# Kernel optimization log

Hardware: AMD Instinct MI355X
Metric: run time of the kernel (lower is better)

The kernel has to match this reference:

```python
import jax, jax.numpy as jnp
import numpy as np

# Model constants (from source: model_dim=1024, head_dim=128, num_heads=8)
L = 8          # num layers (reduced from 16 for tractable reference memory)
T = 2048       # packed tokens, B == 1 (varlen)
DIM = 1024
NH = 8
NKV = 4        # GQA kv heads
HD = 128
KVD = NKV * HD
BLOCK = 128
WS = 3
WIN = WS * BLOCK           # sliding-window size for 'S' layers
ATTN_SCALE = 0.12
PATTERN = 'SSSL'
GATE_CH = 32
EPS = 1.1920929e-07        # torch F.rms_norm default eps = finfo(fp32).eps


def rms_norm(x):
    return x * jax.lax.rsqrt(jnp.mean(x * x, axis=-1, keepdims=True) + EPS)


def apply_rotary(x, cos, sin):
    # x: [T, H, HD]; cos/sin: [T, 1, HD//2]
    d = x.shape[-1] // 2
    x1, x2 = x[..., :d], x[..., d:]
    return jnp.concatenate([x1 * cos + x2 * sin, -x1 * sin + x2 * cos], axis=-1)


def has_ve(layer_idx, n_layer):
    return layer_idx % 2 == (n_layer - 1) % 2


def setup_inputs() -> dict:
    key = jax.random.key(0)
    ks = jax.random.split(key, 9)
    x = jax.random.normal(ks[0], (1, T, DIM), jnp.float32)
    ve = jax.random.normal(ks[1], (L, T, KVD), jnp.float32)
    s = DIM ** -0.5
    Wq = jax.random.normal(ks[2], (L, DIM, NH * HD), jnp.float32) * s
    Wk = jax.random.normal(ks[3], (L, DIM, KVD), jnp.float32) * s
    Wv = jax.random.normal(ks[4], (L, DIM, KVD), jnp.float32) * s
    Wo = jax.random.normal(ks[5], (L, NH * HD, DIM), jnp.float32) * (NH * HD) ** -0.5
    Wgate = jax.random.normal(ks[6], (L, GATE_CH, NKV), jnp.float32) * GATE_CH ** -0.5
    Wfc = jax.random.normal(ks[7], (L, DIM, 4 * DIM), jnp.float32) * s
    Wproj = jax.random.normal(ks[8], (L, 4 * DIM, DIM), jnp.float32) * (4 * DIM) ** -0.5
    # RoPE tables (absolute positions of the packed batch, as in the source)
    inv_freq = 1.0 / (10000.0 ** (jnp.arange(HD // 2, dtype=jnp.float32) / (HD // 2)))
    ang = jnp.arange(T, dtype=jnp.float32)[:, None] * inv_freq[None, :]
    cos = jnp.cos(ang)[:, None, :]
    sin = jnp.sin(ang)[:, None, :]
    # cu_seqlens: 4 packed documents of 512 tokens
    seqlens = jnp.array([0, 512, 1024, 1536, 2048], dtype=jnp.int32)
    return dict(x=x, ve=ve, Wq=Wq, Wk=Wk, Wv=Wv, Wo=Wo, Wgate=Wgate,
                Wfc=Wfc, Wproj=Wproj, cos=cos, sin=sin, seqlens=seqlens)


def reference(x, ve, Wq, Wk, Wv, Wo, Wgate, Wfc, Wproj, cos, sin, seqlens):
    h = x[0]  # [T, DIM], B == 1 (varlen packing)
    pos = jnp.arange(T)
    doc = jnp.searchsorted(seqlens, pos, side='right') - 1
    diff = pos[:, None] - pos[None, :]
    base = (diff >= 0) & (doc[:, None] == doc[None, :])   # causal within doc
    mask_S = base & (diff <= WIN)                         # sliding window
    neg = jnp.float32(-1e30)
    rep = NH // NKV
    for l in range(L):
        xn = rms_norm(h)
        q = (xn @ Wq[l]).reshape(T, NH, HD)
        k = (xn @ Wk[l]).reshape(T, NKV, HD)
        v = (xn @ Wv[l]).reshape(T, NKV, HD)
        if has_ve(l, L):
            gate = 2.0 * jax.nn.sigmoid(xn[:, :GATE_CH] @ Wgate[l])  # [T, NKV]
            v = v + gate[:, :, None] * ve[l].reshape(T, NKV, HD)
        q = rms_norm(apply_rotary(q, cos, sin))
        k = rms_norm(apply_rotary(k, cos, sin))
        k = jnp.repeat(k, rep, axis=1)   # GQA -> full heads
        v2 = jnp.repeat(v, rep, axis=1)
        scores = jnp.einsum('thd,shd->hts', q, k) * ATTN_SCALE  # [NH, T, T]
        mask = mask_S if PATTERN[l % len(PATTERN)] == 'S' else base
        scores = jnp.where(mask[None], scores, neg)
        p = jax.nn.softmax(scores, axis=-1)
        y = jnp.einsum('hts,shd->thd', p, v2).reshape(T, NH * HD)
        h = h + y @ Wo[l]
        m = jnp.square(jax.nn.relu(rms_norm(h) @ Wfc[l]))  # relu(x)^2 MLP
        h = h + m @ Wproj[l]
    return h[None]
```

## Files before the change

kernel.cpp:

```cpp
#include <hip/hip_runtime.h>
#include <hip/hip_bf16.h>
#include <cstdint>
#include <cstddef>

#define TT     2048
#define DMODEL 1024
#define NHQ    8
#define HD     128
#define KVD    512
#define WIN    384
#define EPSF   1.1920929e-07f
#define SCALE  0.12f

typedef __attribute__((ext_vector_type(8))) short bf16x8;
typedef __attribute__((ext_vector_type(4))) float f32x4;

#define WAITV(N)  asm volatile("s_waitcnt vmcnt(" #N ")" ::: "memory")

__device__ __forceinline__ float b2f(unsigned short u) {
    unsigned int i = ((unsigned int)u) << 16; float f; __builtin_memcpy(&f, &i, 4); return f;
}
__device__ __forceinline__ unsigned short f2b(float f) {
    unsigned int i; __builtin_memcpy(&i, &f, 4);
    unsigned int r = (i + 0x7fffu + ((i >> 16) & 1u)) >> 16;
    return (unsigned short)r;
}

__device__ __forceinline__ void gl_lds16(const unsigned short* g, unsigned short* l) {
    __builtin_amdgcn_global_load_lds(
        (const __attribute__((address_space(1))) unsigned int*)g,
        (__attribute__((address_space(3))) unsigned int*)l, 16, 0, 0);
}
__device__ __forceinline__ void gl_lds16f(const float* g, float* l) {
    __builtin_amdgcn_global_load_lds(
        (const __attribute__((address_space(1))) unsigned int*)g,
        (__attribute__((address_space(3))) unsigned int*)l, 16, 0, 0);
}

__global__ __launch_bounds__(512)
void convT_k(const float* __restrict__ Wq, const float* __restrict__ Wk,
             const float* __restrict__ Wv, const float* __restrict__ Wo,
             const float* __restrict__ Wfc, const float* __restrict__ Wproj,
             unsigned short* __restrict__ Bqkv, unsigned short* __restrict__ Bo,
             unsigned short* __restrict__ Bfc, unsigned short* __restrict__ Bproj)
{
    __shared__ float lt[128 * 128];
    const int bid = blockIdx.x, tid = threadIdx.x, l = blockIdx.y;

    const float* W; unsigned short* Wt; int K, N, t, nbase;
    if (bid < 64)         { W = Wq    + (size_t)l * 1024 * 1024; Wt = Bqkv  + (size_t)l * 2048 * 1024; K = 1024; N = 1024; t = bid;       nbase = 0;    }
    else if (bid < 96)    { W = Wk    + (size_t)l * 1024 * 512;  Wt = Bqkv  + (size_t)l * 2048 * 1024; K = 1024; N = 512;  t = bid - 64;  nbase = 1024; }
    else if (bid < 128)   { W = Wv    + (size_t)l * 1024 * 512;  Wt = Bqkv  + (size_t)l * 2048 * 1024; K = 1024; N = 512;  t = bid - 96;  nbase = 1536; }
    else if (bid < 192)   { W = Wo    + (size_t)l * 1024 * 1024; Wt = Bo    + (size_t)l * 1024 * 1024; K = 1024; N = 1024; t = bid - 128; nbase = 0;    }
    else if (bid < 448)   { W = Wfc   + (size_t)l * 1024 * 4096; Wt = Bfc   + (size_t)l * 4096 * 1024; K = 1024; N = 4096; t = bid - 192; nbase = 0;    }
    else                  { W = Wproj + (size_t)l * 4096 * 1024; Wt = Bproj + (size_t)l * 1024 * 4096; K = 4096; N = 1024; t = bid - 448; nbase = 0;    }

    const int ktiles = K >> 7;
    const int kt0 = (t % ktiles) * 128, nt0 = (t / ktiles) * 128;

    const int lane = tid & 63, w = tid >> 6;
    const int lhi = lane >> 5;
    const int lc  = lane & 31;

    #pragma unroll
    for (int rd = 0; rd < 8; ++rd) {
        const int k = rd * 16 + w * 2 + lhi;
        const int csrc = lc ^ ((k >> 3) & 31);
        const float* src = W + (size_t)(kt0 + k) * N + nt0 + csrc * 4;
        float* dst = lt + (size_t)(rd * 16 + w * 2) * 128;
        gl_lds16f(src, dst);
    }
    __syncthreads();

    #pragma unroll
    for (int i = 0; i < 4; ++i) {
        int flat = i * 512 + tid;
        int n = flat >> 4, kc = (flat & 15) * 8;
        const int c = ((n >> 2) ^ (kc >> 3)) & 31;
        const float* rp = lt + (size_t)kc * 128 + c * 4 + (n & 3);
        unsigned short o[8];
        #pragma unroll
        for (int j = 0; j < 8; ++j) o[j] = f2b(rp[j * 128]);
        *(uint4*)(Wt + (size_t)(nbase + nt0 + n) * K + kt0 + kc) = *(const uint4*)o;
    }
}

template<int EPI>
__global__ __launch_bounds__(256, 2)
void gemm4(const unsigned short* __restrict__ A, const unsigned short* __restrict__ Bt,
           unsigned short* __restrict__ Cp, int K, int ksplit, int Ntot)
{
    __shared__ unsigned short As[2 * 128 * 64];
    __shared__ unsigned short Bs[2 * 128 * 64];
    const int BUF = 128 * 64;
    const int tid = threadIdx.x, lane = tid & 63, wv = tid >> 6;

    const int gx = gridDim.x;
    const int nwg = gx * gridDim.y;
    const int ihw = blockIdx.y * gx + blockIdx.x;
    const int q = nwg >> 3, r = nwg & 7;
    const int xcd = ihw & 7, pos = ihw >> 3;
    const int lg = (xcd < r) ? xcd * (q + 1) + pos
                             : r * (q + 1) + (xcd - r) * q + pos;
    const int m0 = (lg % gx) * 128, n0 = (lg / gx) * 128;

    const int kbeg = blockIdx.z * ksplit;
    const int NT = ksplit >> 6;

    const int wr = (wv >> 1) * 64, wc = (wv & 1) * 64;
    const int l15 = lane & 15, g = lane >> 4;
    const int srow = lane >> 3;
    const int sxor = (((lane & 7) ^ srow) << 3);

    const unsigned short* gA0 = A  + (size_t)(m0 + wv * 32 + srow) * K + sxor;
    const unsigned short* gB0 = Bt + (size_t)(n0 + wv * 32 + srow) * K + sxor;

    auto stage = [&](int t) {
        const int b = t & 1;
        const size_t k = (size_t)kbeg + ((size_t)t << 6);
        unsigned short* la = As + b * BUF + (wv * 32) * 64;
        unsigned short* lb = Bs + b * BUF + (wv * 32) * 64;
        #pragma unroll
        for (int c = 0; c < 4; ++c) {
            gl_lds16(gA0 + (size_t)(c * 8) * K + k, la + c * 8 * 64);
            gl_lds16(gB0 + (size_t)(c * 8) * K + k, lb + c * 8 * 64);
        }
    };

    f32x4 acc[4][4] = {};

    stage(0);
    for (int t = 0; t < NT; ++t) {
        if (t + 1 < NT) { stage(t + 1); WAITV(8); }
        else            { WAITV(0); }
        __builtin_amdgcn_s_barrier();

        const unsigned short* Ac = As + (t & 1) * BUF;
        const unsigned short* Bc = Bs + (t & 1) * BUF;
        bf16x8 af[4][2], bfv[4][2];
        #pragma unroll
        for (int mi = 0; mi < 4; ++mi) {
            const int row = wr + mi * 16 + l15, x = row & 7;
            #pragma unroll
            for (int kk = 0; kk < 2; ++kk)
                af[mi][kk] = *(const bf16x8*)(Ac + row * 64 + (((kk * 4 + g) ^ x) << 3));
        }
        #pragma unroll
        for (int ni = 0; ni < 4; ++ni) {
            const int row = wc + ni * 16 + l15, x = row & 7;
            #pragma unroll
            for (int kk = 0; kk < 2; ++kk)
                bfv[ni][kk] = *(const bf16x8*)(Bc + row * 64 + (((kk * 4 + g) ^ x) << 3));
        }
        __builtin_amdgcn_s_setprio(1);
        #pragma unroll
        for (int kk = 0; kk < 2; ++kk)
            #pragma unroll
            for (int mi = 0; mi < 4; ++mi)
                #pragma unroll
                for (int ni = 0; ni < 4; ++ni)
                    acc[mi][ni] = __builtin_amdgcn_mfma_f32_16x16x32_bf16(af[mi][kk], bfv[ni][kk], acc[mi][ni], 0, 0, 0);
        __builtin_amdgcn_s_setprio(0);
        __builtin_amdgcn_s_barrier();
    }

    const int lr4 = (lane >> 4) * 4;
    unsigned short* Cz = Cp + (size_t)blockIdx.z * TT * Ntot;
    #pragma unroll
    for (int mi = 0; mi < 4; ++mi)
        #pragma unroll
        for (int ni = 0; ni < 4; ++ni)
            #pragma unroll
            for (int r2 = 0; r2 < 4; ++r2) {
                int row = m0 + wr + mi * 16 + lr4 + r2;
                int col = n0 + wc + ni * 16 + l15;
                size_t idx = (size_t)row * Ntot + col;
                float v = acc[mi][ni][r2];
                if (EPI == 0) Cz[idx] = f2b(v);
                else {
                    float z = v > 0.f ? v * v : 0.f;
                    Cz[idx] = f2b(z);
                }
            }
}

__global__ __launch_bounds__(256)
void rmsnormF_k(float* __restrict__ h, const unsigned short* __restrict__ part, int nz,
                unsigned short* __restrict__ xn)
{
    const int t = blockIdx.x, tid = threadIdx.x;
    const size_t idx = (size_t)t * (DMODEL / 4) + tid;
    float4 v = ((const float4*)h)[idx];
    for (int z = 0; z < nz; ++z) {
        ushort4 p = ((const ushort4*)part)[idx + (size_t)z * (TT * DMODEL / 4)];
        v.x += b2f(p.x); v.y += b2f(p.y); v.z += b2f(p.z); v.w += b2f(p.w);
    }
    if (nz > 0) ((float4*)h)[idx] = v;

    float ss = v.x*v.x + v.y*v.y + v.z*v.z + v.w*v.w;
    #pragma unroll
    for (int m = 1; m < 64; m <<= 1) ss += __shfl_xor(ss, m);
    __shared__ float red[4];
    if ((tid & 63) == 0) red[tid >> 6] = ss;
    __syncthreads();
    float tot = red[0] + red[1] + red[2] + red[3];
    float rs = rsqrtf(tot * (1.f / DMODEL) + EPSF);
    unsigned short o[4] = { f2b(v.x*rs), f2b(v.y*rs), f2b(v.z*rs), f2b(v.w*rs) };
    *(ushort4*)(xn + (size_t)t * DMODEL + tid * 4) = *(const ushort4*)o;
}

__global__ __launch_bounds__(256)
void reduce_add_k(float* __restrict__ h, const unsigned short* __restrict__ part, int nz)
{
    const int i = blockIdx.x * 256 + threadIdx.x;
    float4 hv = ((float4*)h)[i];
    for (int z = 0; z < nz; ++z) {
        ushort4 p = ((const ushort4*)part)[i + (size_t)z * (TT * DMODEL / 4)];
        hv.x += b2f(p.x); hv.y += b2f(p.y); hv.z += b2f(p.z); hv.w += b2f(p.w);
    }
    ((float4*)h)[i] = hv;
}

__global__ __launch_bounds__(256)
void post_qkv_k(const unsigned short* __restrict__ qkv, const unsigned short* __restrict__ xn,
                const float* __restrict__ cosb, const float* __restrict__ sinb,
                const float* __restrict__ Wgate, const float* __restrict__ vel, int hasve,
                unsigned short* __restrict__ qn, unsigned short* __restrict__ kn,
                unsigned short* __restrict__ vrow)
{
    const size_t S2 = (size_t)TT * 2048;
    const int t = blockIdx.x, tid = threadIdx.x;
    __shared__ float cs[64], sn[64], gate[4];
    if (tid < 64) { cs[tid] = cosb[t * 64 + tid]; sn[tid] = sinb[t * 64 + tid]; }
    if (hasve && tid >= 64 && tid < 68) {
        int g = tid - 64; float a = 0.f;
        for (int c = 0; c < 32; ++c) a += b2f(xn[(size_t)t * DMODEL + c]) * Wgate[c * 4 + g];
        gate[g] = 2.f / (1.f + __expf(-a));
    }
    __syncthreads();
    if (tid < 96) {
        const int hid = tid >> 3, sub = tid & 7;
        const unsigned short* src; unsigned short* dst;
        if (hid < 8) { src = qkv + (size_t)t * 2048 + hid * 128;              dst = qn + (size_t)t * 1024 + hid * 128; }
        else         { src = qkv + (size_t)t * 2048 + 1024 + (hid - 8) * 128; dst = kn + (size_t)t * 512 + (hid - 8) * 128; }
        float o1[8], o2[8], ssum = 0.f;
        #pragma unroll
        for (int j = 0; j < 8; ++j) {
            int jj = sub * 8 + j;
            float x1 = b2f(src[jj])      + b2f(src[jj + S2]);
            float x2 = b2f(src[jj + 64]) + b2f(src[jj + 64 + S2]);
            float c = cs[jj], s = sn[jj];
            o1[j] = x1 * c + x2 * s;
            o2[j] = -x1 * s + x2 * c;
            ssum += o1[j]*o1[j] + o2[j]*o2[j];
        }
        ssum += __shfl_xor(ssum, 1); ssum += __shfl_xor(ssum, 2); ssum += __shfl_xor(ssum, 4);
        float rs = rsqrtf(ssum * (1.f / HD) + EPSF);
        #pragma unroll
        for (int j = 0; j < 8; ++j) {
            int jj = sub * 8 + j;
            dst[jj]      = f2b(o1[j] * rs);
            dst[jj + 64] = f2b(o2[j] * rs);
        }
    }
    {
        int d0 = tid * 2;
        #pragma unroll
        for (int j = 0; j < 2; ++j) {
            int d = d0 + j;
            size_t off = (size_t)t * 2048 + 1536 + d;
            float vv = b2f(qkv[off]) + b2f(qkv[off + S2]);
            if (hasve) vv += gate[d >> 7] * vel[(size_t)t * KVD + d];
            vrow[(size_t)t * KVD + d] = f2b(vv);
        }
    }
}

__global__ __launch_bounds__(256)
void vtrans_k(const unsigned short* __restrict__ vrow, unsigned short* __restrict__ vt)
{
    __shared__ unsigned short lt[64][72];
    const int t0 = blockIdx.x * 64, c0 = blockIdx.y * 64, tid = threadIdx.x;
    #pragma unroll
    for (int i = 0; i < 2; ++i) {
        int r = (tid >> 3) + i * 32;
        int c = (tid & 7) * 8;
        bf16x8 v = *(const bf16x8*)(vrow + (size_t)(t0 + r) * KVD + c0 + c);
        #pragma unroll
        for (int j = 0; j < 8; ++j) lt[c + j][r] = ((unsigned short*)&v)[j];
    }
    __syncthreads();
    #pragma unroll
    for (int i = 0; i < 2; ++i) {
        int r = (tid >> 3) + i * 32;
        int c = (tid & 7) * 8;
        *(bf16x8*)(vt + (size_t)(c0 + r) * TT + t0 + c) = *(const bf16x8*)(&lt[r][c]);
    }
}

__global__ __launch_bounds__(256)
void attn_k(const unsigned short* __restrict__ qn, const unsigned short* __restrict__ kn,
            const unsigned short* __restrict__ vt, unsigned short* __restrict__ y,
            const int* __restrict__ seqlens, int isS)
{
    __shared__ float Ot[4][16][132];
    const int tid = threadIdx.x, w = tid >> 6, lane = tid & 63;
    const int h = blockIdx.y, hkv = h >> 1;
    const int qr = (blockIdx.x * 4 + w) * 16;
    const int s1 = seqlens[1], s2 = seqlens[2], s3 = seqlens[3];
    const int l15 = lane & 15, g = lane >> 4;

    bf16x8 qf[4];
    #pragma unroll
    for (int kk = 0; kk < 4; ++kk)
        qf[kk] = *(const bf16x8*)(qn + (size_t)(qr + l15) * 1024 + h * HD + kk * 32 + g * 8);

    const int row = qr + l15;
    const int drow = (row >= s1) + (row >= s2) + (row >= s3);

    int dq = (qr >= s1) + (qr >= s2) + (qr >= s3);
    int dstart = dq == 0 ? 0 : (dq == 1 ? s1 : (dq == 2 ? s2 : s3));
    int smin = dstart;
    if (isS) { int wlo = qr - WIN; if (wlo > smin) smin = wlo; }
    if (smin < 0) smin = 0;
    const int smax = qr + 16;

    f32x4 acc[8] = {};
    float mrow = -1e30f, lrow = 0.f;

    for (int s0 = smin & ~31; s0 < smax; s0 += 32) {
        f32x4 S[2] = {};
        __builtin_amdgcn_s_setprio(1);
        #pragma unroll
        for (int nb = 0; nb < 2; ++nb) {
            int srow = s0 + nb * 16 + l15;
            #pragma unroll
            for (int kk = 0; kk < 4; ++kk) {
                bf16x8 kf = *(const bf16x8*)(kn + (size_t)srow * KVD + hkv * HD + kk * 32 + g * 8);
                S[nb] = __builtin_amdgcn_mfma_f32_16x16x32_bf16(kf, qf[kk], S[nb], 0, 0, 0);
            }
        }
        __builtin_amdgcn_s_setprio(0);

        float sv[2][4];
        #pragma unroll
        for (int nb = 0; nb < 2; ++nb)
            #pragma unroll
            for (int r = 0; r < 4; ++r) {
                int s = s0 + nb * 16 + 4 * g + r;
                int dcol = (s >= s1) + (s >= s2) + (s >= s3);
                bool valid = (s <= row) && (dcol == drow) && (!isS || (row - s) <= WIN);
                sv[nb][r] = valid ? S[nb][r] * SCALE : -1e30f;
            }

        float pm = sv[0][0];
        #pragma unroll
        for (int r = 1; r < 4; ++r) pm = fmaxf(pm, sv[0][r]);
        #pragma unroll
        for (int r = 0; r < 4; ++r) pm = fmaxf(pm, sv[1][r]);
        pm = fmaxf(pm, __shfl_xor(pm, 16));
        pm = fmaxf(pm, __shfl_xor(pm, 32));
        float mnew = fmaxf(mrow, pm);
        float scl2 = __expf(mrow - mnew);
        float p0[4], p1[4], ps = 0.f;
        #pragma unroll
        for (int r = 0; r < 4; ++r) {
            p0[r] = __expf(sv[0][r] - mnew);
            p1[r] = __expf(sv[1][r] - mnew);
            ps += p0[r] + p1[r];
        }
        ps += __shfl_xor(ps, 16);
        ps += __shfl_xor(ps, 32);
        lrow = lrow * scl2 + ps;
        mrow = mnew;
        #pragma unroll
        for (int nb2 = 0; nb2 < 8; ++nb2) acc[nb2] *= scl2;

        unsigned short pt[8];
        const int base = l15 + ((g & 1) << 5);
        #pragma unroll
        for (int jh = 0; jh < 2; ++jh)
            #pragma unroll
            for (int r = 0; r < 4; ++r) {
                float ta = __shfl(p0[r], base + 16 * jh);
                float tb = __shfl(p1[r], base + 16 * jh);
                pt[jh * 4 + r] = f2b(g >= 2 ? tb : ta);
            }
        bf16x8 pf;
        #pragma unroll
        for (int j = 0; j < 8; ++j) ((unsigned short*)&pf)[j] = pt[j];

        __builtin_amdgcn_s_setprio(1);
        #pragma unroll
        for (int nb2 = 0; nb2 < 8; ++nb2) {
            bf16x8 vf = *(const bf16x8*)(vt + (size_t)(hkv * HD + nb2 * 16 + l15) * TT + s0 + g * 8);
            acc[nb2] = __builtin_amdgcn_mfma_f32_16x16x32_bf16(vf, pf, acc[nb2], 0, 0, 0);
        }
        __builtin_amdgcn_s_setprio(0);
    }

    const float inv = 1.f / lrow;
    #pragma unroll
    for (int nb2 = 0; nb2 < 8; ++nb2)
        #pragma unroll
        for (int r = 0; r < 4; ++r)
            Ot[w][l15][nb2 * 16 + 4 * g + r] = acc[nb2][r] * inv;
    __syncthreads();
    const int qo = lane >> 2, dblk = (lane & 3) * 32;
    #pragma unroll
    for (int i4 = 0; i4 < 4; ++i4) {
        unsigned short ob[8];
        #pragma unroll
        for (int j = 0; j < 8; ++j) ob[j] = f2b(Ot[w][qo][dblk + i4 * 8 + j]);
        *(uint4*)(y + (size_t)(qr + qo) * 1024 + h * HD + dblk + i4 * 8) = *(const uint4*)ob;
    }
}

extern "C" void kernel_launch(void* const* d_in, const int* in_sizes, int n_in,
                              void* d_out, int out_size, void* d_ws, size_t ws_size,
                              hipStream_t stream)
{
    const float* x       = (const float*)d_in[0];
    const float* ve      = (const float*)d_in[1];
    const float* Wq      = (const float*)d_in[2];
    const float* Wk      = (const float*)d_in[3];
    const float* Wv      = (const float*)d_in[4];
    const float* Wo      = (const float*)d_in[5];
    const float* Wgate   = (const float*)d_in[6];
    const float* Wfc     = (const float*)d_in[7];
    const float* Wproj   = (const float*)d_in[8];
    const float* cosb    = (const float*)d_in[9];
    const float* sinb    = (const float*)d_in[10];
    const int*   seqlens = (const int*)d_in[11];

    float* h = (float*)d_out;
    char* ws = (char*)d_ws;
    unsigned short* xn    = (unsigned short*)(ws);
    unsigned short* qn    = (unsigned short*)(ws + (4ull  << 20));
    unsigned short* kn    = (unsigned short*)(ws + (8ull  << 20));
    unsigned short* vrow  = (unsigned short*)(ws + (10ull << 20));
    unsigned short* vt    = (unsigned short*)(ws + (12ull << 20));
    unsigned short* yb    = (unsigned short*)(ws + (14ull << 20));
    unsigned short* mb    = (unsigned short*)(ws + (18ull << 20));
    unsigned short* part  = (unsigned short*)(ws + (34ull << 20));
    unsigned short* Bqkv  = (unsigned short*)(ws + (50ull  << 20));
    unsigned short* Bo    = (unsigned short*)(ws + (82ull  << 20));
    unsigned short* Bfc   = (unsigned short*)(ws + (98ull  << 20));
    unsigned short* Bproj = (unsigned short*)(ws + (162ull << 20));

    hipMemcpyAsync(h, x, (size_t)TT * DMODEL * sizeof(float), hipMemcpyDeviceToDevice, stream);

    convT_k<<<dim3(704, 8), 512, 0, stream>>>(Wq, Wk, Wv, Wo, Wfc, Wproj,
                                              Bqkv, Bo, Bfc, Bproj);

    for (int l = 0; l < 8; ++l) {
        int hasve = (l % 2) == 1;
        int isS   = (l % 4) != 3;

        rmsnormF_k<<<TT, 256, 0, stream>>>(h, part, l == 0 ? 0 : 4, xn);

        gemm4<0><<<dim3(16, 16, 2), 256, 0, stream>>>(xn, Bqkv + (size_t)l * 2048 * 1024,
                                                      part, 1024, 512, 2048);

        post_qkv_k<<<TT, 256, 0, stream>>>(part, xn, cosb, sinb,
            Wgate + (size_t)l * 128, ve + (size_t)l * TT * KVD, hasve, qn, kn, vrow);

        vtrans_k<<<dim3(32, 8), 256, 0, stream>>>(vrow, vt);

        attn_k<<<dim3(32, 8), 256, 0, stream>>>(qn, kn, vt, yb, seqlens, isS);

        gemm4<0><<<dim3(16, 8, 4), 256, 0, stream>>>(yb, Bo + (size_t)l * 1024 * 1024,
                                                     part, 1024, 256, 1024);

        rmsnormF_k<<<TT, 256, 0, stream>>>(h, part, 4, xn);

        gemm4<2><<<dim3(16, 32, 1), 256, 0, stream>>>(xn, Bfc + (size_t)l * 4096 * 1024,
                                                      mb, 1024, 1024, 4096);

        gemm4<0><<<dim3(16, 8, 4), 256, 0, stream>>>(mb, Bproj + (size_t)l * 1024 * 4096,
                                                     part, 4096, 1024, 1024);
    }

    reduce_add_k<<<2048, 256, 0, stream>>>(h, part, 4);
}
```

Before: 1.388 ms.

## Add 256x128-tile 8-wave GEMM kernel for the MLP fc and proj matmuls

Adds a new gemm9 kernel that uses 512-thread workgroups and 256x128 output tiles, double-buffered in LDS. The A tile is staged in two 128-row halves interleaved with the MFMA compute, and workgroups are remapped so neighbouring tiles land on the same XCD. The MLP up-projection and down-projection now launch through it instead of gemm4. The aim is more data reuse per tile and better overlap of global loads with compute. The cost is higher register and LDS use, which leaves one workgroup per CU, and only half as many workgroups per launch.

```diff
diff --git a/kernel.cpp b/kernel.cpp
--- a/kernel.cpp
+++ b/kernel.cpp
@@ -164,7 +164,6 @@
         __builtin_amdgcn_s_barrier();
     }
 
-    const int lr4 = (lane >> 4) * 4;
     unsigned short* Cz = Cp + (size_t)blockIdx.z * TT * Ntot;
     #pragma unroll
     for (int mi = 0; mi < 4; ++mi)
@@ -172,8 +171,142 @@
         for (int ni = 0; ni < 4; ++ni)
             #pragma unroll
             for (int r2 = 0; r2 < 4; ++r2) {
-                int row = m0 + wr + mi * 16 + lr4 + r2;
+                int row = m0 + wr + mi * 16 + g * 4 + r2;
                 int col = n0 + wc + ni * 16 + l15;
+                size_t idx = (size_t)row * Ntot + col;
+                float v = acc[mi][ni][r2];
+                if (EPI == 0) Cz[idx] = f2b(v);
+                else {
+                    float z = v > 0.f ? v * v : 0.f;
+                    Cz[idx] = f2b(z);
+                }
+            }
+}
+
+template<int EPI>
+__global__ __launch_bounds__(512, 1)
+void gemm9(const unsigned short* __restrict__ A, const unsigned short* __restrict__ Bt,
+           unsigned short* __restrict__ Cp, int K, int ksplit, int Ntot)
+{
+    __shared__ unsigned short As[2 * 2 * 128 * 64];
+    __shared__ unsigned short Bs[2 * 128 * 64];
+    const int HBUF = 128 * 64;
+    const int tid = threadIdx.x, lane = tid & 63, wv = tid >> 6;
+    const int wm = wv >> 2, wn = wv & 3;
+
+    const int gx = gridDim.x;
+    const int nwg = gx * gridDim.y;
+    const int ihw = blockIdx.y * gx + blockIdx.x;
+    const int q = nwg >> 3, r = nwg & 7;
+    const int xcd = ihw & 7, pos = ihw >> 3;
+    const int lg = (xcd < r) ? xcd * (q + 1) + pos
+                             : r * (q + 1) + (xcd - r) * q + pos;
+    const int m0 = (lg % gx) * 256, n0 = (lg / gx) * 128;
+
+    const int kbeg = blockIdx.z * ksplit;
+    const int NT = ksplit >> 6;
+
+    const int l15 = lane & 15, g = lane >> 4;
+    const int srow = tid >> 3;
+    const int sxor = (((tid & 7) ^ (srow & 7)) << 3);
+
+    const unsigned short* gA = A  + (size_t)(m0 + srow) * K + sxor;
+    const unsigned short* gB = Bt + (size_t)(n0 + srow) * K + sxor;
+
+    auto stageA = [&](int t, int mh) {
+        const int buf = t & 1;
+        const size_t kof = (size_t)kbeg + ((size_t)t << 6);
+        #pragma unroll
+        for (int c = 0; c < 2; ++c) {
+            const unsigned short* src = gA + (size_t)(mh * 128 + c * 64) * K + kof;
+            unsigned short* dst = As + buf * (2 * HBUF) + mh * HBUF + (c * 64 + wv * 8) * 64;
+            gl_lds16(src, dst);
+        }
+    };
+    auto stageB = [&](int t) {
+        const int buf = t & 1;
+        const size_t kof = (size_t)kbeg + ((size_t)t << 6);
+        #pragma unroll
+        for (int c = 0; c < 2; ++c) {
+            const unsigned short* src = gB + (size_t)(c * 64) * K + kof;
+            unsigned short* dst = Bs + buf * HBUF + (c * 64 + wv * 8) * 64;
+            gl_lds16(src, dst);
+        }
+    };
+
+    f32x4 acc[8][2] = {};
+    bf16x8 afr[4][2], bfr[2][2];
+
+    stageA(0, 0);
+    stageB(0);
+    stageA(0, 1);
+
+    for (int t = 0; t < NT; ++t) {
+        const bool more = (t + 1 < NT);
+        const unsigned short* Ab = As + (t & 1) * (2 * HBUF);
+        const unsigned short* Bb = Bs + (t & 1) * HBUF;
+
+        if (more) { stageA(t + 1, 0); stageB(t + 1); WAITV(6); }
+        else      { WAITV(2); }
+        __builtin_amdgcn_s_barrier();
+
+        #pragma unroll
+        for (int mi2 = 0; mi2 < 4; ++mi2) {
+            const int row = mi2 * 32 + wm * 16 + l15, x = l15 & 7;
+            #pragma unroll
+            for (int kk = 0; kk < 2; ++kk)
+                afr[mi2][kk] = *(const bf16x8*)(Ab + row * 64 + (((kk * 4 + g) ^ x) << 3));
+        }
+        #pragma unroll
+        for (int ni = 0; ni < 2; ++ni) {
+            const int row = wn * 32 + ni * 16 + l15, x = l15 & 7;
+            #pragma unroll
+            for (int kk = 0; kk < 2; ++kk)
+                bfr[ni][kk] = *(const bf16x8*)(Bb + row * 64 + (((kk * 4 + g) ^ x) << 3));
+        }
+        __builtin_amdgcn_s_setprio(1);
+        #pragma unroll
+        for (int kk = 0; kk < 2; ++kk)
+            #pragma unroll
+            for (int mi2 = 0; mi2 < 4; ++mi2)
+                #pragma unroll
+                for (int ni = 0; ni < 2; ++ni)
+                    acc[mi2][ni] = __builtin_amdgcn_mfma_f32_16x16x32_bf16(afr[mi2][kk], bfr[ni][kk], acc[mi2][ni], 0, 0, 0);
+        __builtin_amdgcn_s_setprio(0);
+        __builtin_amdgcn_s_barrier();
+
+        if (more) { stageA(t + 1, 1); WAITV(6); }
+        else      { WAITV(0); }
+        __builtin_amdgcn_s_barrier();
+
+        #pragma unroll
+        for (int mi2 = 0; mi2 < 4; ++mi2) {
+            const int row = mi2 * 32 + wm * 16 + l15, x = l15 & 7;
+            #pragma unroll
+            for (int kk = 0; kk < 2; ++kk)
+                afr[mi2][kk] = *(const bf16x8*)(Ab + HBUF + row * 64 + (((kk * 4 + g) ^ x) << 3));
+        }
+        __builtin_amdgcn_s_setprio(1);
+        #pragma unroll
+        for (int kk = 0; kk < 2; ++kk)
+            #pragma unroll
+            for (int mi2 = 0; mi2 < 4; ++mi2)
+                #pragma unroll
+                for (int ni = 0; ni < 2; ++ni)
+                    acc[4 + mi2][ni] = __builtin_amdgcn_mfma_f32_16x16x32_bf16(afr[mi2][kk], bfr[ni][kk], acc[4 + mi2][ni], 0, 0, 0);
+        __builtin_amdgcn_s_setprio(0);
+        __builtin_amdgcn_s_barrier();
+    }
+
+    unsigned short* Cz = Cp + (size_t)blockIdx.z * TT * Ntot;
+    #pragma unroll
+    for (int mi = 0; mi < 8; ++mi)
+        #pragma unroll
+        for (int ni = 0; ni < 2; ++ni)
+            #pragma unroll
+            for (int r2 = 0; r2 < 4; ++r2) {
+                int row = m0 + (mi >> 2) * 128 + (mi & 3) * 32 + wm * 16 + g * 4 + r2;
+                int col = n0 + wn * 32 + ni * 16 + l15;
                 size_t idx = (size_t)row * Ntot + col;
                 float v = acc[mi][ni][r2];
                 if (EPI == 0) Cz[idx] = f2b(v);
@@ -474,11 +607,11 @@
 
         rmsnormF_k<<<TT, 256, 0, stream>>>(h, part, 4, xn);
 
-        gemm4<2><<<dim3(16, 32, 1), 256, 0, stream>>>(xn, Bfc + (size_t)l * 4096 * 1024,
-                                                      mb, 1024, 1024, 4096);
-
-        gemm4<0><<<dim3(16, 8, 4), 256, 0, stream>>>(mb, Bproj + (size_t)l * 1024 * 4096,
-                                                     part, 4096, 1024, 1024);
+        gemm9<2><<<dim3(8, 32, 1), 512, 0, stream>>>(xn, Bfc + (size_t)l * 4096 * 1024,
+                                                     mb, 1024, 1024, 4096);
+
+        gemm9<0><<<dim3(8, 8, 4), 512, 0, stream>>>(mb, Bproj + (size_t)l * 1024 * 4096,
+                                                    part, 4096, 1024, 1024);
     }
 
     reduce_add_k<<<2048, 256, 0, stream>>>(h, part, 4);
```

Result: slower. 1.521 ms (+9.6%).
